# Optimization experiments

Hardware: AMD Instinct MI355X
Metric: run time of the kernel (lower is better)

Reference implementation:

```python
import jax, jax.numpy as jnp
import numpy as np

S, B, D, H = 2048, 2, 2048, 16
HD = D // H  # 128
EPS = 1e-5


def _layernorm(x, w, b):
    mu = jnp.mean(x, axis=-1, keepdims=True)
    var = jnp.mean((x - mu) ** 2, axis=-1, keepdims=True)
    return (x - mu) * jax.lax.rsqrt(var + EPS) * w + b


def _apply_rotary(x, freqs_cis):
    # x: [B, S, H, HD]; freqs_cis: [S, HD//2, 2]
    xr = x.astype(jnp.float32).reshape(x.shape[0], x.shape[1], x.shape[2], HD // 2, 2)
    f = freqs_cis.reshape(1, xr.shape[1], 1, xr.shape[3], 2)
    out = jnp.stack(
        [xr[..., 0] * f[..., 0] - xr[..., 1] * f[..., 1],
         xr[..., 1] * f[..., 0] + xr[..., 0] * f[..., 1]],
        axis=-1,
    )
    return out.reshape(x.shape).astype(x.dtype)


def setup_inputs() -> dict:
    key = jax.random.key(0)
    ks = jax.random.split(key, 6)
    scale = 0.02
    return {
        "x": jax.random.normal(ks[0], (S, B, D), dtype=jnp.float32),
        "freqs_cis": jax.random.normal(ks[1], (S, HD // 2, 2), dtype=jnp.float32),
        "wqkv_w": jax.random.normal(ks[2], (3 * D, D), dtype=jnp.float32) * scale,
        "wqkv_b": jnp.zeros((3 * D,), dtype=jnp.float32),
        "wo_w": jax.random.normal(ks[3], (D, D), dtype=jnp.float32) * scale,
        "wo_b": jnp.zeros((D,), dtype=jnp.float32),
        "qn_w": jnp.ones((HD,), dtype=jnp.float32),
        "qn_b": jnp.zeros((HD,), dtype=jnp.float32),
        "kn_w": jnp.ones((HD,), dtype=jnp.float32),
        "kn_b": jnp.zeros((HD,), dtype=jnp.float32),
    }


def reference(x, freqs_cis, wqkv_w, wqkv_b, wo_w, wo_b, qn_w, qn_b, kn_w, kn_b):
    # x: [S, B, D] -> [B, S, D]
    xb = jnp.transpose(x, (1, 0, 2))
    qkv = jnp.einsum("bsd,ed->bse", xb, wqkv_w) + wqkv_b  # [B, S, 3D]
    xq, xk, xv = jnp.split(qkv, 3, axis=-1)
    xq = xq.reshape(B, S, H, HD)
    xk = xk.reshape(B, S, H, HD)
    xv = xv.reshape(B, S, H, HD)
    # QK-norm over head_dim
    xq = _layernorm(xq, qn_w, qn_b)
    xk = _layernorm(xk, kn_w, kn_b)
    # RoPE
    xq = _apply_rotary(xq, freqs_cis)
    xk = _apply_rotary(xk, freqs_cis)
    # [B, H, S, HD]
    q = jnp.transpose(xq, (0, 2, 1, 3))
    k = jnp.transpose(xk, (0, 2, 1, 3))
    v = jnp.transpose(xv, (0, 2, 1, 3))
    scores = jnp.einsum("bhqd,bhkd->bhqk", q, k) / jnp.sqrt(jnp.float32(HD))
    causal = jnp.tril(jnp.ones((S, S), dtype=bool))
    scores = jnp.where(causal, scores, jnp.finfo(scores.dtype).min)
    attn = jax.nn.softmax(scores, axis=-1)
    out = jnp.einsum("bhqk,bhkd->bhqd", attn, v)  # [B, H, S, HD]
    out = jnp.transpose(out, (0, 2, 1, 3)).reshape(B, S, D)
    out = jnp.einsum("bsd,ed->bse", out, wo_w) + wo_b
    return jnp.transpose(out, (1, 0, 2))  # [S, B, D]
```

## Files before the change

kernel.cpp:

```cpp
#include <hip/hip_runtime.h>
#include <hip/hip_bf16.h>

#define S 2048
#define B 2
#define D 2048
#define H 16
#define HD 128
#define N3 6144
#define KD 2048

typedef __hip_bfloat16 bf16;
typedef float f32x4 __attribute__((ext_vector_type(4)));
typedef short short8 __attribute__((ext_vector_type(8)));
typedef short sv4 __attribute__((ext_vector_type(4)));

__device__ __forceinline__ void gload16(const void* g, void* l) {
    __builtin_amdgcn_global_load_lds((const __attribute__((address_space(1))) void*)g,
                                     (__attribute__((address_space(3))) void*)l, 16, 0, 0);
}
__device__ __forceinline__ void bar() {
    asm volatile("" ::: "memory");
    __builtin_amdgcn_s_barrier();
    asm volatile("" ::: "memory");
}

__device__ __forceinline__ short8 cvt8(const float* p) {
    f32x4 a = *(const f32x4*)p;
    f32x4 b = *(const f32x4*)(p + 4);
    short8 r;
#pragma unroll
    for (int j = 0; j < 4; ++j) {
        __hip_bfloat16 t0 = __float2bfloat16(a[j]);
        __hip_bfloat16 t1 = __float2bfloat16(b[j]);
        r[j]     = reinterpret_cast<short&>(t0);
        r[j + 4] = reinterpret_cast<short&>(t1);
    }
    return r;
}

__global__ __launch_bounds__(256) void cvt_x_kernel(const float* __restrict__ x, bf16* __restrict__ xb) {
    int i = (blockIdx.x * 256 + threadIdx.x) * 8;
    int d  = i & (D - 1);
    int sb = i >> 11;
    int b  = sb & (B - 1);
    int s  = sb >> 1;
    *(short8*)&xb[((size_t)(b * S + s) << 11) + d] = cvt8(x + i);
}

__global__ __launch_bounds__(256) void cvt_w_kernel(const float* __restrict__ in, bf16* __restrict__ o, int n) {
    for (int i = (blockIdx.x * blockDim.x + threadIdx.x) * 8; i < n; i += gridDim.x * blockDim.x * 8)
        *(short8*)&o[i] = cvt8(in + i);
}

template <int MODE>
__global__ __launch_bounds__(256, 2) void gemm128(
    const bf16* __restrict__ A, const bf16* __restrict__ W, const float* __restrict__ bias,
    bf16* __restrict__ oq, bf16* __restrict__ ok, bf16* __restrict__ ovT,
    float* __restrict__ oOut)
{
    constexpr int NT = KD / 64;

    __shared__ __align__(16) bf16 SA[2][128 * 64];
    __shared__ __align__(16) bf16 SB[2][128 * 64];

    const int tid = threadIdx.x;
    const int w = tid >> 6, l = tid & 63;
    const int wm = w >> 1, wn = w & 1;
    const int l15 = l & 15, l4 = l >> 4;

    const int id  = blockIdx.y * gridDim.x + blockIdx.x;
    const int xcd = id & 7;
    const int j   = id >> 3;
    const int npx = gridDim.x >> 3;
    const int tileN = (xcd * npx + j % npx) * 128;
    const int tileM = (j / npx) * 128;

    const int lrow8 = l >> 3;
    const int lsb   = ((l & 7) * 16) ^ (lrow8 << 4);
    const int rxor  = (l15 & 7) << 3;

    const char* AgT = (const char*)A + (size_t)tileM * (KD * 2);
    const char* WgT = (const char*)W + (size_t)tileN * (KD * 2);

    auto stage_tile = [&](int buf, int kt) {
#pragma unroll
        for (int j2 = 0; j2 < 4; ++j2) {
            const int chunk = w * 4 + j2;
            gload16(AgT + (size_t)(chunk * 8 + lrow8) * (KD * 2) + kt * 128 + lsb,
                    (char*)&SA[buf][0] + chunk * 1024);
        }
#pragma unroll
        for (int j2 = 0; j2 < 4; ++j2) {
            const int chunk = w * 4 + j2;
            gload16(WgT + (size_t)(chunk * 8 + lrow8) * (KD * 2) + kt * 128 + lsb,
                    (char*)&SB[buf][0] + chunk * 1024);
        }
    };

    f32x4 acc[4][4] = {};

#define TILE_BODY(BUF, KTN)                                                                \
    {                                                                                      \
        stage_tile(BUF ^ 1, KTN);                                                          \
        _Pragma("unroll") for (int kk = 0; kk < 2; ++kk) {                                 \
            short8 bfrag[4], afr[4];                                                       \
            _Pragma("unroll") for (int ni = 0; ni < 4; ++ni)                               \
                bfrag[ni] = *(const short8*)&SB[BUF][(wn * 64 + ni * 16 + l15) * 64 +      \
                                                     ((kk * 32 + l4 * 8) ^ rxor)];         \
            _Pragma("unroll") for (int q = 0; q < 4; ++q)                                  \
                afr[q] = *(const short8*)&SA[BUF][(wm * 64 + q * 16 + l15) * 64 +          \
                                                  ((kk * 32 + l4 * 8) ^ rxor)];            \
            __builtin_amdgcn_s_setprio(1);                                                 \
            _Pragma("unroll") for (int q = 0; q < 4; ++q)                                  \
                _Pragma("unroll") for (int ni = 0; ni < 4; ++ni)                           \
                    acc[q][ni] = __builtin_amdgcn_mfma_f32_16x16x32_bf16(                  \
                        afr[q], bfrag[ni], acc[q][ni], 0, 0, 0);                           \
            __builtin_amdgcn_s_setprio(0);                                                 \
        }                                                                                  \
        asm volatile("s_waitcnt vmcnt(0)" ::: "memory");                                   \
        bar();                                                                             \
    }

    stage_tile(0, 0);
    asm volatile("s_waitcnt vmcnt(0)" ::: "memory");
    bar();

#pragma unroll 1
    for (int t = 0; t < NT; t += 2) {
        const int tn1 = (t + 1 < NT) ? t + 1 : NT - 1;
        const int tn2 = (t + 2 < NT) ? t + 2 : NT - 1;
        TILE_BODY(0, tn1)
        TILE_BODY(1, tn2)
    }
#undef TILE_BODY

#pragma unroll
    for (int mi = 0; mi < 4; ++mi) {
#pragma unroll
        for (int ni = 0; ni < 4; ++ni) {
            const int ncol = tileN + wn * 64 + ni * 16 + l15;
            const float bv = bias[ncol];
            const int m0 = tileM + wm * 64 + mi * 16 + l4 * 4;
            if (MODE == 0) {
                const int b_ = m0 >> 11, s0 = m0 & (S - 1);
                const int which = ncol >> 11;
                const int hh = (ncol >> 7) & (H - 1);
                const int hd = ncol & (HD - 1);
                const int bh = b_ * H + hh;
                if (which == 2) {
                    sv4 pk;
#pragma unroll
                    for (int r = 0; r < 4; ++r) {
                        __hip_bfloat16 t = __float2bfloat16(acc[mi][ni][r] + bv);
                        pk[r] = reinterpret_cast<short&>(t);
                    }
                    *(sv4*)&ovT[((size_t)bh * HD + hd) * S + s0] = pk;
                } else {
                    bf16* dst = which ? ok : oq;
#pragma unroll
                    for (int r = 0; r < 4; ++r)
                        dst[((size_t)bh * S + s0 + r) * HD + hd] =
                            __float2bfloat16(acc[mi][ni][r] + bv);
                }
            } else {
#pragma unroll
                for (int r = 0; r < 4; ++r) {
                    const int m = m0 + r;
                    const int b_ = m >> 11, s_ = m & (S - 1);
                    oOut[((size_t)s_ * B + b_) * D + ncol] = acc[mi][ni][r] + bv;
                }
            }
        }
    }
}

__global__ __launch_bounds__(256) void ln_rope_kernel(
    bf16* __restrict__ q, bf16* __restrict__ k,
    const float* __restrict__ fc,
    const float* __restrict__ qw, const float* __restrict__ qb,
    const float* __restrict__ kw, const float* __restrict__ kb)
{
    const int tid = threadIdx.x;
    const int w = tid >> 6, l = tid & 63;
    const int row = blockIdx.x * 4 + w;
    const int s_ = row & (S - 1);
    const size_t base = (size_t)row * HD;
    const float f0 = fc[s_ * HD + 2 * l];
    const float f1 = fc[s_ * HD + 2 * l + 1];

#pragma unroll
    for (int which = 0; which < 2; ++which) {
        bf16* p = which == 0 ? q : k;
        const float* gw = which == 0 ? qw : kw;
        const float* gb = which == 0 ? qb : kb;
        const float osc = which == 0 ? 0.08838834764831845f : 1.0f;
        float x0 = __bfloat162float(p[base + 2 * l]);
        float x1 = __bfloat162float(p[base + 2 * l + 1]);
        float sm = x0 + x1;
#pragma unroll
        for (int msk = 1; msk < 64; msk <<= 1) sm += __shfl_xor(sm, msk);
        const float mu = sm * (1.0f / HD);
        const float d0 = x0 - mu, d1 = x1 - mu;
        float vs = d0 * d0 + d1 * d1;
#pragma unroll
        for (int msk = 1; msk < 64; msk <<= 1) vs += __shfl_xor(vs, msk);
        const float rstd = rsqrtf(vs * (1.0f / HD) + 1e-5f);
        const float n0 = d0 * rstd * gw[2 * l] + gb[2 * l];
        const float n1 = d1 * rstd * gw[2 * l + 1] + gb[2 * l + 1];
        p[base + 2 * l]     = __float2bfloat16((n0 * f0 - n1 * f1) * osc);
        p[base + 2 * l + 1] = __float2bfloat16((n1 * f0 + n0 * f1) * osc);
    }
}

__global__ __launch_bounds__(256, 2) void attn_kernel(
    const bf16* __restrict__ q, const bf16* __restrict__ k, const bf16* __restrict__ vT,
    bf16* __restrict__ out)
{
    __shared__ __align__(16) bf16 KT[2][64 * 128];
    __shared__ __align__(16) bf16 VS[2][128 * 64];
    __shared__ __align__(16) bf16 Pb[4][16 * 72];

    const int tid = threadIdx.x, w = tid >> 6, l = tid & 63;
    const int l15 = l & 15, l4 = l >> 4;

    const int id  = blockIdx.y * gridDim.x + blockIdx.x;
    const int nid = (id & 7) * 64 + (id >> 3);
    const int bh  = nid >> 4;
    const int pr  = nid & 15;
    const int qtA = 31 - pr;
    const int qtB = pr;

    const int b_ = bh >> 4, hh = bh & (H - 1);
    const int qrA = qtA * 64 + w * 16;
    const int qrB = qtB * 64 + w * 16;
    const size_t hQ = (size_t)bh * S * HD;
    const size_t hV = (size_t)bh * HD * S;

    const char* kbase = (const char*)(k + hQ);
    const char* vbase = (const char*)(vT + hV);
    int ksrc[4], vsrc[4], kdst[4], vdst[4];
#pragma unroll
    for (int j = 0; j < 4; ++j) {
        const int ik = w * 4 + j;
        const int rt = ik * 4 + (l >> 4);
        ksrc[j] = rt * 256 + (((l & 15) * 16) ^ ((rt & 15) << 4));
        kdst[j] = ik * 1024;
        const int rd = ik * 8 + (l >> 3);
        vsrc[j] = rd * (S * 2) + (((l & 7) * 16) ^ ((rd & 7) << 4));
        vdst[j] = ik * 1024;
    }

    short8 aqA[4], aqB[4];
#pragma unroll
    for (int c = 0; c < 4; ++c) {
        aqA[c] = *(const short8*)&q[hQ + (size_t)(qrA + l15) * HD + c * 32 + l4 * 8];
        aqB[c] = *(const short8*)&q[hQ + (size_t)(qrB + l15) * HD + c * 32 + l4 * 8];
    }

    f32x4 oA[8] = {}, oB[8] = {};
    float psA[4] = {0.f, 0.f, 0.f, 0.f}, psB[4] = {0.f, 0.f, 0.f, 0.f};

#pragma unroll
    for (int j = 0; j < 4; ++j)
        gload16(kbase + ksrc[j], (char*)KT[0] + kdst[j]);

    const int kx = l15 << 3;
    const int vx = (l15 & 7) << 3;
    const float LOG2E = 1.4426950408889634f;
    const float SHIFT = -23.083120654223414f;

    for (int kvt = 0; kvt <= qtA; ++kvt) {
        const int kvb = kvt * 64;
        const int cur = kvt & 1;
        const bool doB = (kvt <= qtB);
#pragma unroll
        for (int j = 0; j < 4; ++j)
            gload16(vbase + (size_t)kvb * 2 + vsrc[j], (char*)VS[cur] + vdst[j]);
        if (kvt < qtA) {
#pragma unroll
            for (int j = 0; j < 4; ++j)
                gload16(kbase + (size_t)(kvb + 64) * 256 + ksrc[j], (char*)KT[cur ^ 1] + kdst[j]);
        }
        if (kvt < qtA) { asm volatile("s_waitcnt vmcnt(8)" ::: "memory"); }
        else           { asm volatile("s_waitcnt vmcnt(4)" ::: "memory"); }
        bar();

        short8 apA[2], apB[2];
        {
            f32x4 sacc[4] = {};
#pragma unroll
            for (int c = 0; c < 4; ++c) {
                const int cole = (c * 32 + l4 * 8) ^ kx;
#pragma unroll
                for (int n = 0; n < 4; ++n) {
                    short8 bk = *(const short8*)&KT[cur][(n * 16 + l15) * 128 + cole];
                    sacc[n] = __builtin_amdgcn_mfma_f32_16x16x32_bf16(aqA[c], bk, sacc[n], 0, 0, 0);
                }
            }
            if (kvt == qtA) {
#pragma unroll
                for (int n = 0; n < 4; ++n)
#pragma unroll
                    for (int r = 0; r < 4; ++r) {
                        float sv = (kvb + n * 16 + l15 > qrA + l4 * 4 + r) ? -1e30f : sacc[n][r];
                        const float pv = __builtin_amdgcn_exp2f(__builtin_fmaf(sv, LOG2E, SHIFT));
                        sacc[n][r] = pv; psA[r] += pv;
                    }
            } else {
#pragma unroll
                for (int n = 0; n < 4; ++n)
#pragma unroll
                    for (int r = 0; r < 4; ++r) {
                        const float pv = __builtin_amdgcn_exp2f(__builtin_fmaf(sacc[n][r], LOG2E, SHIFT));
                        sacc[n][r] = pv; psA[r] += pv;
                    }
            }
#pragma unroll
            for (int n = 0; n < 4; ++n)
#pragma unroll
                for (int r = 0; r < 4; ++r)
                    Pb[w][(l4 * 4 + r) * 72 + n * 16 + l15] = __float2bfloat16(sacc[n][r]);
#pragma unroll
            for (int c = 0; c < 2; ++c)
                apA[c] = *(const short8*)&Pb[w][l15 * 72 + c * 32 + l4 * 8];
        }
        if (doB) {
            f32x4 sacc[4] = {};
#pragma unroll
            for (int c = 0; c < 4; ++c) {
                const int cole = (c * 32 + l4 * 8) ^ kx;
#pragma unroll
                for (int n = 0; n < 4; ++n) {
                    short8 bk = *(const short8*)&KT[cur][(n * 16 + l15) * 128 + cole];
                    sacc[n] = __builtin_amdgcn_mfma_f32_16x16x32_bf16(aqB[c], bk, sacc[n], 0, 0, 0);
                }
            }
            if (kvt == qtB) {
#pragma unroll
                for (int n = 0; n < 4; ++n)
#pragma unroll
                    for (int r = 0; r < 4; ++r) {
                        float sv = (kvb + n * 16 + l15 > qrB + l4 * 4 + r) ? -1e30f : sacc[n][r];
                        const float pv = __builtin_amdgcn_exp2f(__builtin_fmaf(sv, LOG2E, SHIFT));
                        sacc[n][r] = pv; psB[r] += pv;
                    }
            } else {
#pragma unroll
                for (int n = 0; n < 4; ++n)
#pragma unroll
                    for (int r = 0; r < 4; ++r) {
                        const float pv = __builtin_amdgcn_exp2f(__builtin_fmaf(sacc[n][r], LOG2E, SHIFT));
                        sacc[n][r] = pv; psB[r] += pv;
                    }
            }
#pragma unroll
            for (int n = 0; n < 4; ++n)
#pragma unroll
                for (int r = 0; r < 4; ++r)
                    Pb[w][(l4 * 4 + r) * 72 + n * 16 + l15] = __float2bfloat16(sacc[n][r]);
#pragma unroll
            for (int c = 0; c < 2; ++c)
                apB[c] = *(const short8*)&Pb[w][l15 * 72 + c * 32 + l4 * 8];
        }

        if (kvt < qtA) { asm volatile("s_waitcnt vmcnt(4)" ::: "memory"); }
        else           { asm volatile("s_waitcnt vmcnt(0)" ::: "memory"); }
        bar();

#pragma unroll
        for (int c = 0; c < 2; ++c) {
#pragma unroll
            for (int d = 0; d < 8; ++d) {
                const int rd = d * 16 + l15;
                short8 bv = *(const short8*)&VS[cur][rd * 64 + ((c * 32 + l4 * 8) ^ vx)];
                oA[d] = __builtin_amdgcn_mfma_f32_16x16x32_bf16(apA[c], bv, oA[d], 0, 0, 0);
            }
        }
        if (doB) {
#pragma unroll
            for (int c = 0; c < 2; ++c) {
#pragma unroll
                for (int d = 0; d < 8; ++d) {
                    const int rd = d * 16 + l15;
                    short8 bv = *(const short8*)&VS[cur][rd * 64 + ((c * 32 + l4 * 8) ^ vx)];
                    oB[d] = __builtin_amdgcn_mfma_f32_16x16x32_bf16(apB[c], bv, oB[d], 0, 0, 0);
                }
            }
        }
    }

#pragma unroll
    for (int r = 0; r < 4; ++r) {
#pragma unroll
        for (int msk = 1; msk < 16; msk <<= 1) psA[r] += __shfl_xor(psA[r], msk);
        const float inv = 1.0f / psA[r];
        const int s_ = qrA + l4 * 4 + r;
        const size_t obase = ((size_t)b_ * S + s_) * D + hh * HD;
#pragma unroll
        for (int d = 0; d < 8; ++d)
            out[obase + d * 16 + l15] = __float2bfloat16(oA[d][r] * inv);
    }
#pragma unroll
    for (int r = 0; r < 4; ++r) {
#pragma unroll
        for (int msk = 1; msk < 16; msk <<= 1) psB[r] += __shfl_xor(psB[r], msk);
        const float inv = 1.0f / psB[r];
        const int s_ = qrB + l4 * 4 + r;
        const size_t obase = ((size_t)b_ * S + s_) * D + hh * HD;
#pragma unroll
        for (int d = 0; d < 8; ++d)
            out[obase + d * 16 + l15] = __float2bfloat16(oB[d][r] * inv);
    }
}

extern "C" void kernel_launch(void* const* d_in, const int* in_sizes, int n_in,
                              void* d_out, int out_size, void* d_ws, size_t ws_size,
                              hipStream_t stream) {
    const float* x      = (const float*)d_in[0];
    const float* fc     = (const float*)d_in[1];
    const float* wqkv_w = (const float*)d_in[2];
    const float* wqkv_b = (const float*)d_in[3];
    const float* wo_w   = (const float*)d_in[4];
    const float* wo_b   = (const float*)d_in[5];
    const float* qn_w   = (const float*)d_in[6];
    const float* qn_b   = (const float*)d_in[7];
    const float* kn_w   = (const float*)d_in[8];
    const float* kn_b   = (const float*)d_in[9];
    float* out = (float*)d_out;
    char* ws = (char*)d_ws;

    bf16* xb = (bf16*)(ws);
    bf16* w1 = (bf16*)(ws + 16777216);
    bf16* wo = (bf16*)(ws + 41943040);
    bf16* qb = (bf16*)(ws + 50331648);
    bf16* kb = (bf16*)(ws + 67108864);
    bf16* vT = (bf16*)(ws + 83886080);
    bf16* ao = (bf16*)(ws + 100663296);

    cvt_x_kernel<<<(S * B * D) / (256 * 8), 256, 0, stream>>>(x, xb);
    cvt_w_kernel<<<2048, 256, 0, stream>>>(wqkv_w, w1, N3 * D);
    cvt_w_kernel<<<1024, 256, 0, stream>>>(wo_w, wo, D * D);

    gemm128<0><<<dim3(N3 / 128, (B * S) / 128), 256, 0, stream>>>(
        xb, w1, wqkv_b, qb, kb, vT, nullptr);

    ln_rope_kernel<<<(B * H * S) / 4, 256, 0, stream>>>(qb, kb, fc, qn_w, qn_b, kn_w, kn_b);

    attn_kernel<<<dim3(16, B * H), 256, 0, stream>>>(qb, kb, vT, ao);

    gemm128<1><<<dim3(D / 128, (B * S) / 128), 256, 0, stream>>>(
        ao, wo, wo_b, nullptr, nullptr, nullptr, out);
}
```

Before: 251.8 us.

## Single-buffer GEMM LDS: load all fragments to registers, then prefetch next tile

Replaces the double-buffered LDS pipeline in the projection GEMM with a single buffer. Each iteration first reads the whole 64-wide K tile of A/B fragments into registers, barriers, then issues the global-to-LDS load for the next tile while running the MFMAs from registers. This halves LDS usage, which may allow more blocks per CU, at the cost of more fragment registers and an extra barrier per K step.

Result: faster. 232.1 us (median of 2 runs) (-7.8%).

```diff
diff --git a/kernel.cpp b/kernel.cpp
--- a/kernel.cpp
+++ b/kernel.cpp
@@ -60,8 +60,8 @@
 {
     constexpr int NT = KD / 64;
 
-    __shared__ __align__(16) bf16 SA[2][128 * 64];
-    __shared__ __align__(16) bf16 SB[2][128 * 64];
+    __shared__ __align__(16) bf16 SA[128 * 64];
+    __shared__ __align__(16) bf16 SB[128 * 64];
 
     const int tid = threadIdx.x;
     const int w = tid >> 6, l = tid & 63;
@@ -82,57 +82,60 @@
     const char* AgT = (const char*)A + (size_t)tileM * (KD * 2);
     const char* WgT = (const char*)W + (size_t)tileN * (KD * 2);
 
-    auto stage_tile = [&](int buf, int kt) {
+    auto stage_tile = [&](int kt) {
 #pragma unroll
         for (int j2 = 0; j2 < 4; ++j2) {
             const int chunk = w * 4 + j2;
             gload16(AgT + (size_t)(chunk * 8 + lrow8) * (KD * 2) + kt * 128 + lsb,
-                    (char*)&SA[buf][0] + chunk * 1024);
+                    (char*)&SA[0] + chunk * 1024);
         }
 #pragma unroll
         for (int j2 = 0; j2 < 4; ++j2) {
             const int chunk = w * 4 + j2;
             gload16(WgT + (size_t)(chunk * 8 + lrow8) * (KD * 2) + kt * 128 + lsb,
-                    (char*)&SB[buf][0] + chunk * 1024);
+                    (char*)&SB[0] + chunk * 1024);
         }
     };
 
     f32x4 acc[4][4] = {};
 
-#define TILE_BODY(BUF, KTN)                                                                \
-    {                                                                                      \
-        stage_tile(BUF ^ 1, KTN);                                                          \
-        _Pragma("unroll") for (int kk = 0; kk < 2; ++kk) {                                 \
-            short8 bfrag[4], afr[4];                                                       \
-            _Pragma("unroll") for (int ni = 0; ni < 4; ++ni)                               \
-                bfrag[ni] = *(const short8*)&SB[BUF][(wn * 64 + ni * 16 + l15) * 64 +      \
-                                                     ((kk * 32 + l4 * 8) ^ rxor)];         \
-            _Pragma("unroll") for (int q = 0; q < 4; ++q)                                  \
-                afr[q] = *(const short8*)&SA[BUF][(wm * 64 + q * 16 + l15) * 64 +          \
-                                                  ((kk * 32 + l4 * 8) ^ rxor)];            \
-            __builtin_amdgcn_s_setprio(1);                                                 \
-            _Pragma("unroll") for (int q = 0; q < 4; ++q)                                  \
-                _Pragma("unroll") for (int ni = 0; ni < 4; ++ni)                           \
-                    acc[q][ni] = __builtin_amdgcn_mfma_f32_16x16x32_bf16(                  \
-                        afr[q], bfrag[ni], acc[q][ni], 0, 0, 0);                           \
-            __builtin_amdgcn_s_setprio(0);                                                 \
-        }                                                                                  \
-        asm volatile("s_waitcnt vmcnt(0)" ::: "memory");                                   \
-        bar();                                                                             \
-    }
-
-    stage_tile(0, 0);
+    stage_tile(0);
     asm volatile("s_waitcnt vmcnt(0)" ::: "memory");
     bar();
 
 #pragma unroll 1
-    for (int t = 0; t < NT; t += 2) {
-        const int tn1 = (t + 1 < NT) ? t + 1 : NT - 1;
-        const int tn2 = (t + 2 < NT) ? t + 2 : NT - 1;
-        TILE_BODY(0, tn1)
-        TILE_BODY(1, tn2)
-    }
-#undef TILE_BODY
+    for (int t = 0; t < NT; ++t) {
+        short8 bfrag[2][4], afr[2][4];
+#pragma unroll
+        for (int kk = 0; kk < 2; ++kk) {
+#pragma unroll
+            for (int ni = 0; ni < 4; ++ni)
+                bfrag[kk][ni] = *(const short8*)&SB[(wn * 64 + ni * 16 + l15) * 64 +
+                                                   ((kk * 32 + l4 * 8) ^ rxor)];
+#pragma unroll
+            for (int q = 0; q < 4; ++q)
+                afr[kk][q] = *(const short8*)&SA[(wm * 64 + q * 16 + l15) * 64 +
+                                                ((kk * 32 + l4 * 8) ^ rxor)];
+        }
+        asm volatile("s_waitcnt lgkmcnt(0)" ::: "memory");
+        bar();
+
+        if (t + 1 < NT) stage_tile(t + 1);
+
+        __builtin_amdgcn_s_setprio(1);
+#pragma unroll
+        for (int kk = 0; kk < 2; ++kk)
+#pragma unroll
+            for (int q = 0; q < 4; ++q)
+#pragma unroll
+                for (int ni = 0; ni < 4; ++ni)
+                    acc[q][ni] = __builtin_amdgcn_mfma_f32_16x16x32_bf16(
+                        afr[kk][q], bfrag[kk][ni], acc[q][ni], 0, 0, 0);
+        __builtin_amdgcn_s_setprio(0);
+
+        asm volatile("s_waitcnt vmcnt(0)" ::: "memory");
+        bar();
+    }
 
 #pragma unroll
     for (int mi = 0; mi < 4; ++mi) {
```
